# Kernel optimization log

Hardware: AMD Instinct MI355X
Metric: run time of the kernel (lower is better)

The kernel has to match this reference:

```python
import jax, jax.numpy as jnp
import numpy as np

K = 75        # kpoints
L = 8         # number of labels (output_dim)


def _knn_nonconformity(q, t, train_label, k=K, num_labels=L):
    """Brute-force kNN (Euclidean) + distance-weighted nonconformity.
    q: [B, D] queries; t: [N, D] train bank; train_label: [N] int.
    Returns [B, num_labels]: for each class i, sum of 1/dist over the k
    nearest neighbors whose label != i (0 weight for zero distance)."""
    # squared distances [B, N]
    d2 = (jnp.sum(q * q, axis=1, keepdims=True)
          - 2.0 * q @ t.T
          + jnp.sum(t * t, axis=1)[None, :])
    d2 = jnp.maximum(d2, 0.0)
    neg_top, idx = jax.lax.top_k(-d2, k)          # k smallest d2
    dist = jnp.sqrt(jnp.maximum(-neg_top, 0.0))    # [B, k]
    safe = jnp.where(dist > 0, dist, 1.0)
    w = jnp.where(dist > 0, 1.0 / safe, 0.0)       # [B, k]
    mismatch = 1.0 - jax.nn.one_hot(train_label[idx], num_labels, dtype=w.dtype)  # [B,k,L]
    return jnp.einsum('bk,bkl->bl', w, mismatch)


def setup_inputs() -> dict:
    key = jax.random.key(0)
    ks = jax.random.split(key, 12)
    B, N, D, H, C = 1024, 50000, 83, 128, 10000
    s = lambda fan_in: 1.0 / np.sqrt(fan_in)
    return {
        'x': jax.random.normal(ks[0], (B, D), jnp.float32),
        'train_x': jax.random.normal(ks[1], (N, D), jnp.float32),
        'train_label': jax.random.randint(ks[2], (N,), 0, L, jnp.int32),
        'cali': jax.random.uniform(ks[3], (C,), jnp.float32) * 50.0,
        'W1': jax.random.normal(ks[4], (D, H), jnp.float32) * s(D),
        'b1': jnp.zeros((H,), jnp.float32),
        'W2': jax.random.normal(ks[5], (H, H), jnp.float32) * s(H),
        'b2': jnp.zeros((H,), jnp.float32),
        'W3': jax.random.normal(ks[6], (H, H), jnp.float32) * s(H),
        'b3': jnp.zeros((H,), jnp.float32),
        'W4': jax.random.normal(ks[7], (H, L), jnp.float32) * s(H),
        'b4': jnp.zeros((L,), jnp.float32),
    }


def reference(x, train_x, train_label, cali, W1, b1, W2, b2, W3, b3, W4, b4):
    relu = jax.nn.relu
    # query-side MLP (inference: dropout inactive)
    h1 = relu(x @ W1 + b1)
    h2 = relu(h1 @ W2 + b2)
    h3 = relu(h2 @ W3 + b3)
    out = jax.nn.softmax(h3 @ W4 + b4, axis=-1)
    # train-side feature banks (what each kNTree was fit on)
    t1 = relu(train_x @ W1 + b1)
    t2 = relu(t1 @ W2 + b2)
    t3 = relu(t2 @ W3 + b3)
    t4 = jax.nn.softmax(t3 @ W4 + b4, axis=-1)
    # per-layer nonconformity [B, L], summed across the 5 layers
    total = (_knn_nonconformity(x, train_x, train_label)
             + _knn_nonconformity(h1, t1, train_label)
             + _knn_nonconformity(h2, t2, train_label)
             + _knn_nonconformity(h3, t3, train_label)
             + _knn_nonconformity(out, t4, train_label))
    # empirical p-value: fraction of calibration scores >= total nonconformity
    counts = jnp.sum(cali[None, None, :] >= total[:, :, None], axis=-1)  # [B, L]
    return counts.astype(jnp.float32) / cali.shape[0]
```

## Files before the change

### kernel.cpp

```cpp
#include <hip/hip_runtime.h>
#include <math.h>

#define KNN 75
#define NL 8
#define NB 1024
#define NT 50000
#define NT_PAD 50048
#define NCALI 10000
#define KC 32
#define TT 128
#define NTB 391
#define SLOTS 16
#define CAP 6144
#define NSUB 2048
#define NSB 16
#define SSTRIDE 24
#define SOFF 11
#define RSEL 32

#define PB_Q    384
#define PB_BANK 18750
#define PB_W1   48
#define PB_W23  64
#define PREP_BLOCKS (PB_Q+PB_BANK+PB_W1+2*PB_W23)

typedef __attribute__((ext_vector_type(8))) short bf16x8;
typedef __attribute__((ext_vector_type(4))) float f32x4;

__device__ __forceinline__ int swz(int c){ return c + ((c>>5)<<2); }

__device__ __forceinline__ unsigned short f2bf_rn(float x){
  unsigned u = __float_as_uint(x);
  unsigned r = (u + 0x7FFFu + ((u>>16)&1u)) >> 16;
  return (unsigned short)r;
}
__device__ __forceinline__ float bf2f(unsigned short h){
  return __uint_as_float(((unsigned)h)<<16);
}
__device__ __forceinline__ bf16x8 ld8(const unsigned short* p){
  return *(const bf16x8*)p;
}
__device__ __forceinline__ void gl_lds16(const unsigned short* g, unsigned short* l){
  __builtin_amdgcn_global_load_lds(
      (const __attribute__((address_space(1))) void*)g,
      (__attribute__((address_space(3))) void*)l, 16, 0, 0);
}

__device__ __forceinline__ void pad_one(const float* __restrict__ in,
                                        float* __restrict__ out, int M,
                                        int Din, int Dout, int idx){
  if (idx >= M*Dout) return;
  int r = idx / Dout, c = idx - r*Dout;
  out[idx] = (c < Din) ? in[r*Din + c] : 0.f;
}
__device__ __forceinline__ void wsplit_one(const float* __restrict__ W, int kreal,
                                           int dp, unsigned short* __restrict__ WtH,
                                           unsigned short* __restrict__ WtL, int idx){
  int n = idx / dp, k = idx - n*dp;
  float v = (k < kreal) ? W[(size_t)k*128 + n] : 0.f;
  unsigned short h = f2bf_rn(v);
  WtH[idx] = h;
  WtL[idx] = f2bf_rn(v - bf2f(h));
}
__global__ void prep_k(const float* __restrict__ x, float* __restrict__ xq0,
                       const float* __restrict__ txr, float* __restrict__ tbA,
                       const float* __restrict__ W1, unsigned short* wt1H, unsigned short* wt1L,
                       const float* __restrict__ W2, unsigned short* wt2H, unsigned short* wt2L,
                       const float* __restrict__ W3, unsigned short* wt3H, unsigned short* wt3L){
  int b = blockIdx.x, tid = threadIdx.x;
  if (b < PB_Q){
    pad_one(x, xq0, NB, 83, 96, b*256 + tid);
  } else if (b < PB_Q + PB_BANK){
    pad_one(txr, tbA, NT, 83, 96, (b-PB_Q)*256 + tid);
  } else if (b < PB_Q + PB_BANK + PB_W1){
    wsplit_one(W1, 83, 96,  wt1H, wt1L, (b-PB_Q-PB_BANK)*256 + tid);
  } else if (b < PB_Q + PB_BANK + PB_W1 + PB_W23){
    wsplit_one(W2, 128, 128, wt2H, wt2L, (b-PB_Q-PB_BANK-PB_W1)*256 + tid);
  } else {
    wsplit_one(W3, 128, 128, wt3H, wt3L, (b-PB_Q-PB_BANK-PB_W1-PB_W23)*256 + tid);
  }
}

__device__ __forceinline__ void qmlp_layer(
    const float* __restrict__ srcG, int lda,
    float (*H)[132], float (*As)[132], float (*Bs)[148],
    int kchunks, int kreal,
    const float* __restrict__ W, const float* __restrict__ bias,
    float* __restrict__ OutG, int rowBase, int tid)
{
  int r0 = (tid>>4)*8, c0 = (tid&15)*8;
  float acc[8][8];
  #pragma unroll
  for (int i=0;i<8;i++)
    #pragma unroll
    for (int j=0;j<8;j++) acc[i][j]=0.f;

  for (int kc=0;kc<kchunks;kc++){
    { int rr = tid>>3, k4=(tid&7)*4;
      #pragma unroll
      for (int i=0;i<4;i++){
        int row = rr + i*32;
        float4 v;
        if (srcG) v = *(const float4*)&srcG[(size_t)(rowBase+row)*lda + kc*KC + k4];
        else      v = *(const float4*)&H[row][kc*KC + k4];
        As[k4+0][row]=v.x; As[k4+1][row]=v.y; As[k4+2][row]=v.z; As[k4+3][row]=v.w;
      }
    }
    { int kk=tid>>5, c4=(tid&31)*4;
      #pragma unroll
      for (int i=0;i<4;i++){
        int k = kk + i*8, gk = kc*KC + k;
        float4 v = make_float4(0.f,0.f,0.f,0.f);
        if (gk < kreal) v = *(const float4*)&W[(size_t)gk*128 + c4];
        *(float4*)&Bs[k][swz(c4)] = v;
      }
    }
    __syncthreads();
    #pragma unroll 4
    for (int k=0;k<KC;k++){
      float4 a0 = *(const float4*)&As[k][r0];
      float4 a1 = *(const float4*)&As[k][r0+4];
      float4 b0 = *(const float4*)&Bs[k][swz(c0)];
      float4 b1 = *(const float4*)&Bs[k][swz(c0+4)];
      float av[8] = {a0.x,a0.y,a0.z,a0.w,a1.x,a1.y,a1.z,a1.w};
      float bv[8] = {b0.x,b0.y,b0.z,b0.w,b1.x,b1.y,b1.z,b1.w};
      #pragma unroll
      for (int i=0;i<8;i++)
        #pragma unroll
        for (int j=0;j<8;j++) acc[i][j] += av[i]*bv[j];
    }
    __syncthreads();
  }
  float bb[8];
  #pragma unroll
  for (int j=0;j<8;j++) bb[j]=bias[c0+j];
  #pragma unroll
  for (int i=0;i<8;i++){
    int row = r0 + i;
    float o[8];
    #pragma unroll
    for (int j=0;j<8;j++){ float v=acc[i][j]+bb[j]; o[j]=v>0.f?v:0.f; }
    *(float4*)&H[row][c0]   = make_float4(o[0],o[1],o[2],o[3]);
    *(float4*)&H[row][c0+4] = make_float4(o[4],o[5],o[6],o[7]);
    *(float4*)&OutG[(size_t)(rowBase+row)*128 + c0]   = make_float4(o[0],o[1],o[2],o[3]);
    *(float4*)&OutG[(size_t)(rowBase+row)*128 + c0+4] = make_float4(o[4],o[5],o[6],o[7]);
  }
  __syncthreads();
}

__device__ __forceinline__ void qsplit(float (*H)[132],
                                       unsigned short* __restrict__ qh,
                                       unsigned short* __restrict__ ql,
                                       float* __restrict__ qn,
                                       int rowBase, int tid){
  if (tid < 128){
    int gr = rowBase + tid;
    float s = 0.f;
    for (int k=0;k<128;k++){
      float v = H[tid][k];
      s += v*v;
      unsigned short h = f2bf_rn(v);
      qh[(size_t)gr*128 + k] = h;
      ql[(size_t)gr*128 + k] = f2bf_rn(v - bf2f(h));
    }
    qn[gr] = s;
  }
}

__global__ __launch_bounds__(256) void qmlp_k(
    const float* __restrict__ xq0,
    const float* __restrict__ W1, const float* __restrict__ b1,
    const float* __restrict__ W2, const float* __restrict__ b2,
    const float* __restrict__ W3, const float* __restrict__ b3,
    const float* __restrict__ W4, const float* __restrict__ b4,
    float* __restrict__ xq1, float* __restrict__ xq2, float* __restrict__ xq3,
    float* __restrict__ xq4,
    unsigned short* qH1, unsigned short* qL1,
    unsigned short* qH2, unsigned short* qL2,
    unsigned short* qH3, unsigned short* qL3,
    unsigned short* qH4, unsigned short* qL4,
    float* __restrict__ qnb)
{
  __shared__ float As[KC][132];
  __shared__ float Bs[KC][148];
  __shared__ float H[128][132];
  int tid = threadIdx.x;
  int rowBase = blockIdx.x*128;

  qmlp_layer(xq0, 96, H, As, Bs, 3, 83,  W1, b1, xq1, rowBase, tid);
  qsplit(H, qH1, qL1, qnb+1*NB, rowBase, tid);
  qmlp_layer(nullptr, 0, H, As, Bs, 4, 128, W2, b2, xq2, rowBase, tid);
  qsplit(H, qH2, qL2, qnb+2*NB, rowBase, tid);
  qmlp_layer(nullptr, 0, H, As, Bs, 4, 128, W3, b3, xq3, rowBase, tid);
  qsplit(H, qH3, qL3, qnb+3*NB, rowBase, tid);

  float* W4s = (float*)Bs;
  for (int i=tid;i<1024;i+=256) W4s[i]=W4[i];
  __syncthreads();
  if (tid < 128){
    int row = rowBase + tid;
    float v[8];
    #pragma unroll
    for (int c=0;c<8;c++) v[c]=b4[c];
    for (int k=0;k<128;k++){
      float a = H[tid][k];
      #pragma unroll
      for (int c=0;c<8;c++) v[c] += a*W4s[k*8+c];
    }
    float m=-1e30f;
    #pragma unroll
    for (int c=0;c<8;c++) m = v[c]>m ? v[c] : m;
    float s=0.f;
    #pragma unroll
    for (int c=0;c<8;c++){ v[c]=__expf(v[c]-m); s+=v[c]; }
    float inv=1.f/s;
    float* p = &xq4[(size_t)row*32];
    float nn=0.f;
    #pragma unroll
    for (int c=0;c<8;c++){
      float pv = v[c]*inv;
      p[c]=pv;
      nn += pv*pv;
      unsigned short h = f2bf_rn(pv);
      qH4[(size_t)row*32 + c] = h;
      qL4[(size_t)row*32 + c] = f2bf_rn(pv - bf2f(h));
    }
    #pragma unroll
    for (int j=8;j<32;j++){ p[j]=0.f; qH4[(size_t)row*32+j]=0; qL4[(size_t)row*32+j]=0; }
    qnb[4*NB + row] = nn;
  }
}

__global__ void mlp8sm_k(const float* __restrict__ A, const float* __restrict__ W4,
                         const float* __restrict__ b4, float* __restrict__ Out,
                         unsigned short* __restrict__ SH, unsigned short* __restrict__ SL,
                         float* __restrict__ nrm, int M){
  __shared__ float Ws[128*8];
  int tid = threadIdx.x;
  for (int i=tid;i<1024;i+=256) Ws[i]=W4[i];
  __syncthreads();
  int r = blockIdx.x*32 + (tid>>3), c = tid&7;
  if (r >= M) return;
  const float* a = &A[(size_t)r*128];
  float acc = b4[c];
  #pragma unroll 16
  for (int k=0;k<128;k++) acc += a[k]*Ws[k*8+c];
  int lane = tid & 63, base = lane & ~7;
  float v[8];
  #pragma unroll
  for (int j=0;j<8;j++) v[j] = __shfl(acc, base+j, 64);
  float m=-1e30f;
  #pragma unroll
  for (int j=0;j<8;j++) m = v[j]>m ? v[j] : m;
  float s=0.f;
  #pragma unroll
  for (int j=0;j<8;j++){ v[j]=__expf(v[j]-m); s+=v[j]; }
  float inv=1.f/s;
  float nn=0.f;
  #pragma unroll
  for (int j=0;j<8;j++){ float pv=v[j]*inv; v[j]=pv; nn+=pv*pv; }
  float* p = &Out[(size_t)r*32];
  float pv = v[c];
  p[c]    = pv;
  p[8+c]  = 0.f;
  p[16+c] = 0.f;
  p[24+c] = 0.f;
  unsigned short h = f2bf_rn(pv);
  SH[(size_t)r*32 + c]    = h;
  SL[(size_t)r*32 + c]    = f2bf_rn(pv - bf2f(h));
  SH[(size_t)r*32 + 8+c]  = 0; SL[(size_t)r*32 + 8+c]  = 0;
  SH[(size_t)r*32 + 16+c] = 0; SL[(size_t)r*32 + 16+c] = 0;
  SH[(size_t)r*32 + 24+c] = 0; SL[(size_t)r*32 + 24+c] = 0;
  if (c==0) nrm[r] = nn;
}

__global__ void conv_norm_k(
    const float* __restrict__ XA, unsigned short* __restrict__ HA,
    unsigned short* __restrict__ LA, float* __restrict__ nA, int MA,
    const float* __restrict__ XB, unsigned short* __restrict__ HB,
    unsigned short* __restrict__ LB, float* __restrict__ nB, int MB,
    int dp)
{
  int w = threadIdx.x>>6, lane = threadIdx.x&63;
  int row = blockIdx.x*4 + w;
  const float* src; unsigned short* dh; unsigned short* dl; float* nrm;
  if (row < MA){
    src=&XA[(size_t)row*dp]; dh=&HA[(size_t)row*dp]; dl=&LA[(size_t)row*dp]; nrm=&nA[row];
  } else {
    int r2 = row - MA;
    if (r2 >= MB) return;
    src=&XB[(size_t)r2*dp]; dh=&HB[(size_t)r2*dp]; dl=&LB[(size_t)r2*dp]; nrm=&nB[r2];
  }
  float s=0.f;
  for (int c=lane*2; c<dp; c+=128){
    float2 v = *(const float2*)&src[c];
    s += v.x*v.x + v.y*v.y;
    unsigned short h0 = f2bf_rn(v.x), h1 = f2bf_rn(v.y);
    float r0 = v.x - bf2f(h0), r1 = v.y - bf2f(h1);
    ushort2 hh; hh.x=h0; hh.y=h1;
    ushort2 ll; ll.x=f2bf_rn(r0); ll.y=f2bf_rn(r1);
    *(ushort2*)&dh[c]=hh;
    *(ushort2*)&dl[c]=ll;
  }
  #pragma unroll
  for (int off=32;off>0;off>>=1) s += __shfl_down(s, off, 64);
  if (lane==0) *nrm=s;
}

__device__ __forceinline__ void find_bin(int* hist, int* part, int nb, int Krem,
                                         int tid, int* s_B, int* s_lob){
  int ch = nb>>8;
  int base = tid*ch;
  int s=0;
  for (int b=base;b<base+ch;b++) s+=hist[b];
  int lane = tid & 63, wv = tid>>6;
  int v = s;
  #pragma unroll
  for (int off=1; off<64; off<<=1){
    int u = __shfl_up(v, off, 64);
    if (lane >= off) v += u;
  }
  if (lane==63) part[wv] = v;
  __syncthreads();
  int wbase = 0;
  #pragma unroll
  for (int w2=0; w2<4; w2++) wbase += (w2 < wv) ? part[w2] : 0;
  v += wbase;
  int excl = v - s;
  if (v >= Krem && excl < Krem){
    int lob = excl, B = base + ch - 1;
    for (int b=base;b<base+ch;b++){
      if (lob + hist[b] >= Krem){ B=b; break; }
      lob += hist[b];
    }
    *s_B = B; *s_lob = lob;
  }
  if (tid==255 && v < Krem){ *s_B = nb-1; *s_lob = 0; }
  __syncthreads();
}

__global__ __launch_bounds__(256) void sel64_k(const unsigned* __restrict__ skeys,
                                               unsigned* __restrict__ Tthr){
  __shared__ unsigned buf[NSUB];
  __shared__ int hist[2048];
  __shared__ int part[256];
  __shared__ int sB, sLob;
  int tid=threadIdx.x, q=blockIdx.x;
  for (int i=tid;i<NSUB;i+=256) buf[i]=skeys[(size_t)q*NSUB+i];
  int Krem=RSEL;
  for (int i=tid;i<2048;i+=256) hist[i]=0;
  __syncthreads();
  for (int i=tid;i<NSUB;i+=256) atomicAdd(&hist[buf[i]>>21],1);
  __syncthreads();
  find_bin(hist,part,2048,Krem,tid,&sB,&sLob);
  unsigned pre=(unsigned)sB; Krem-=sLob;
  for (int i=tid;i<2048;i+=256) hist[i]=0;
  __syncthreads();
  for (int i=tid;i<NSUB;i+=256){ unsigned k=buf[i]; if ((k>>21)==pre) atomicAdd(&hist[(k>>10)&0x7FFu],1); }
  __syncthreads();
  find_bin(hist,part,2048,Krem,tid,&sB,&sLob);
  pre=(pre<<11)|(unsigned)sB; Krem-=sLob;
  for (int i=tid;i<1024;i+=256) hist[i]=0;
  __syncthreads();
  for (int i=tid;i<NSUB;i+=256){ unsigned k=buf[i]; if ((k>>10)==pre) atomicAdd(&hist[k&0x3FFu],1); }
  __syncthreads();
  find_bin(hist,part,1024,Krem,tid,&sB,&sLob);
  if (tid==0) Tthr[q]=(pre<<10)|(unsigned)sB;
}

#define MFMA_SEC(BHC, BLC, AH, AL)                                               \
  _Pragma("unroll")                                                              \
  for (int tj=0;tj<8;tj++){                                                      \
    int rowB = tj*16 + col;                                                      \
    int sw = (((quad + (rowB>>1)) & 3) << 3);                                    \
    bf16x8 bh = *(const bf16x8*)&(BHC)[rowB*32 + sw];                            \
    bf16x8 bl = *(const bf16x8*)&(BLC)[rowB*32 + sw];                            \
    acc[tj] = __builtin_amdgcn_mfma_f32_16x16x32_bf16(AH, bh, acc[tj], 0,0,0);   \
    acc[tj] = __builtin_amdgcn_mfma_f32_16x16x32_bf16(AH, bl, acc[tj], 0,0,0);   \
    acc[tj] = __builtin_amdgcn_mfma_f32_16x16x32_bf16(AL, bh, acc[tj], 0,0,0);   \
  }

#define MFMA_KLOOP(ROWMAP)                                                       \
  size_t aoff = (size_t)(qbase + w*16 + col)*dp + quad*8;                        \
  const unsigned short* pAH = QH + aoff;                                         \
  const unsigned short* pAL = QL + aoff;                                         \
  int i0 = tid,      row0 = i0>>2, sg0 = ((i0&3) - (row0>>1)) & 3;               \
  int i1 = tid+256,  row1 = i1>>2, sg1 = ((i1&3) - (row1>>1)) & 3;               \
  size_t g0 = (size_t)(ROWMAP(n0+row0))*dp + (size_t)sg0*8;                      \
  size_t g1 = (size_t)(ROWMAP(n0+row1))*dp + (size_t)sg1*8;                      \
  f32x4 acc[8];                                                                  \
  _Pragma("unroll")                                                              \
  for (int tj=0;tj<8;tj++){ f32x4 z={0.f,0.f,0.f,0.f}; acc[tj]=z; }              \
  gl_lds16(TH + g0, BH0 + i0*8);                                                 \
  gl_lds16(TH + g1, BH0 + i1*8);                                                 \
  gl_lds16(TL + g0, BL0 + i0*8);                                                 \
  gl_lds16(TL + g1, BL0 + i1*8);                                                 \
  bf16x8 xh = ld8(pAH), xl = ld8(pAL);                                           \
  bf16x8 yh = xh, yl = xl;                                                       \
  _Pragma("unroll")                                                              \
  for (int kc=0; kc<kchunks; kc+=2){                                             \
    __syncthreads();                                                             \
    if (kc+1 < kchunks){                                                         \
      size_t ko=(size_t)(kc+1)*32;                                               \
      gl_lds16(TH + g0 + ko, BH1 + i0*8);                                        \
      gl_lds16(TH + g1 + ko, BH1 + i1*8);                                        \
      gl_lds16(TL + g0 + ko, BL1 + i0*8);                                        \
      gl_lds16(TL + g1 + ko, BL1 + i1*8);                                        \
      yh = ld8(pAH + ko); yl = ld8(pAL + ko);                                    \
    }                                                                            \
    MFMA_SEC(BH0, BL0, xh, xl);                                                  \
    if (kc+1 < kchunks){                                                         \
      __syncthreads();                                                           \
      if (kc+2 < kchunks){                                                       \
        size_t ko=(size_t)(kc+2)*32;                                             \
        gl_lds16(TH + g0 + ko, BH0 + i0*8);                                      \
        gl_lds16(TH + g1 + ko, BH0 + i1*8);                                      \
        gl_lds16(TL + g0 + ko, BL0 + i0*8);                                      \
        gl_lds16(TL + g1 + ko, BL0 + i1*8);                                      \
        xh = ld8(pAH + ko); xl = ld8(pAL + ko);                                  \
      }                                                                          \
      MFMA_SEC(BH1, BL1, yh, yl);                                                \
    }                                                                            \
  }

#define ROW_ID(r) (r)
#define ROW_SUB(r) ((r)*SSTRIDE + SOFF)

template<int KCH>
__global__ __launch_bounds__(256) void dist_mfma_k(
    const unsigned short* __restrict__ QH, const unsigned short* __restrict__ QL,
    const unsigned short* __restrict__ TH, const unsigned short* __restrict__ TL,
    const float* __restrict__ qn, const float* __restrict__ tn,
    const int* __restrict__ labels, const unsigned* __restrict__ Tthr,
    unsigned* __restrict__ slab)
{
  constexpr int dp = KCH*32;
  __shared__ __align__(16) unsigned short smem[4*4096];
  unsigned short* BH0 = smem;
  unsigned short* BH1 = smem + 4096;
  unsigned short* BL0 = smem + 8192;
  unsigned short* BL1 = smem + 12288;
  unsigned (*hitbuf)[SLOTS] = (unsigned (*)[SLOTS])smem;
  int* hcnt = (int*)(smem + 4096);
  int b = blockIdx.x;
  int xcd = b & 7, s = b >> 3;
  int qb = s & 15, tslot = s >> 4;
  int t_blk = xcd + 8*tslot;
  if (t_blk >= NTB) return;
  int tid = threadIdx.x, w = tid>>6, lane = tid&63;
  int quad = lane>>4, col = lane&15;
  int qbase = qb*64;
  int n0 = t_blk*TT;
  constexpr int kchunks = KCH;

  MFMA_KLOOP(ROW_ID)

  __syncthreads();
  if (tid<64) hcnt[tid]=0;
  __syncthreads();
  float qnr[4]; unsigned Tq[4]; float thrF[4];
  #pragma unroll
  for (int r=0;r<4;r++){
    int q = qbase + w*16 + quad*4 + r;
    qnr[r]  = qn[q];
    Tq[r]   = Tthr[q];
    thrF[r] = __uint_as_float(Tq[r] | 7u);
  }
  #pragma unroll
  for (int tj=0;tj<8;tj++){
    int t = n0 + tj*16 + col;
    if (t < NT){
      float tnv = tn[t];
      unsigned lab = (unsigned)labels[t];
      #pragma unroll
      for (int r=0;r<4;r++){
        float d2 = fmaf(-2.f, acc[tj][r], qnr[r] + tnv);
        if (d2 <= thrF[r]){
          float d2c = fmaxf(d2, 0.f);
          unsigned key = (__float_as_uint(d2c)&0xFFFFFFF8u) | lab;
          if (key < Tq[r]){
            int ql = w*16 + quad*4 + r;
            int idx = atomicAdd(&hcnt[ql], 1);
            if (idx < SLOTS-1) hitbuf[ql][1+idx] = key;
          }
        }
      }
    }
  }
  __syncthreads();
  if (tid<64) hitbuf[tid][0]=(unsigned)hcnt[tid];
  __syncthreads();
  {
    int q = tid>>2, sub = (tid&3)*4;
    uint4 v = *(uint4*)&hitbuf[q][sub];
    *(uint4*)&slab[((size_t)(qbase+q)*NTB + t_blk)*SLOTS + sub] = v;
  }
}

template<int KCH>
__global__ __launch_bounds__(256) void dist_sub_k(
    const unsigned short* __restrict__ QH, const unsigned short* __restrict__ QL,
    const unsigned short* __restrict__ TH, const unsigned short* __restrict__ TL,
    const float* __restrict__ qn, const float* __restrict__ tn,
    const int* __restrict__ labels, unsigned* __restrict__ keys)
{
  constexpr int dp = KCH*32;
  __shared__ __align__(16) unsigned short smem[4*4096];
  unsigned short* BH0 = smem;
  unsigned short* BH1 = smem + 4096;
  unsigned short* BL0 = smem + 8192;
  unsigned short* BL1 = smem + 12288;
  int b = blockIdx.x;
  int qb = b & 15, t_blk = b >> 4;
  int tid = threadIdx.x, w = tid>>6, lane = tid&63;
  int quad = lane>>4, col = lane&15;
  int qbase = qb*64;
  int n0 = t_blk*TT;
  constexpr int kchunks = KCH;

  MFMA_KLOOP(ROW_SUB)

  float qnr[4];
  #pragma unroll
  for (int r=0;r<4;r++)
    qnr[r] = qn[qbase + w*16 + quad*4 + r];
  #pragma unroll
  for (int tj=0;tj<8;tj++){
    int sI = n0 + tj*16 + col;
    int g  = sI*SSTRIDE + SOFF;
    float tnv = tn[g];
    unsigned lab = (unsigned)labels[g];
    #pragma unroll
    for (int r=0;r<4;r++){
      float d2 = fmaxf(fmaf(-2.f, acc[tj][r], qnr[r] + tnv), 0.f);
      unsigned key = (__float_as_uint(d2)&0xFFFFFFF8u) | lab;
      int q = qbase + w*16 + quad*4 + r;
      keys[(size_t)q*NSUB + sI] = key;
    }
  }
}

template<int KCH>
__global__ __launch_bounds__(256) void mlp_mfma_k(
    const unsigned short* __restrict__ QH, const unsigned short* __restrict__ QL,
    const unsigned short* __restrict__ TH, const unsigned short* __restrict__ TL,
    const float* __restrict__ bias, float* __restrict__ Out,
    unsigned short* __restrict__ SH, unsigned short* __restrict__ SL,
    float* __restrict__ nrm, int M)
{
  constexpr int dp = KCH*32;
  __shared__ __align__(16) unsigned short smem[4*4096];
  unsigned short* BH0 = smem;
  unsigned short* BH1 = smem + 4096;
  unsigned short* BL0 = smem + 8192;
  unsigned short* BL1 = smem + 12288;
  int tid = threadIdx.x, w = tid>>6, lane = tid&63;
  int quad = lane>>4, col = lane&15;
  int qbase = blockIdx.x*64;
  int n0 = 0;
  constexpr int kchunks = KCH;

  MFMA_KLOOP(ROW_ID)

  float bb[8];
  #pragma unroll
  for (int tj=0;tj<8;tj++) bb[tj] = bias[tj*16 + col];
  #pragma unroll
  for (int r=0;r<4;r++){
    int row = qbase + w*16 + quad*4 + r;
    if (row < M){
      float vv[8]; float s=0.f;
      #pragma unroll
      for (int tj=0;tj<8;tj++){
        float v = acc[tj][r] + bb[tj];
        v = v > 0.f ? v : 0.f;
        vv[tj] = v;
        s += v*v;
        Out[(size_t)row*128 + tj*16 + col] = v;
      }
      #pragma unroll
      for (int off=1; off<16; off<<=1) s += __shfl_xor(s, off, 16);
      if (col==0) nrm[row] = s;
      #pragma unroll
      for (int tj=0;tj<8;tj++){
        unsigned short h = f2bf_rn(vv[tj]);
        SH[(size_t)row*128 + tj*16 + col] = h;
        SL[(size_t)row*128 + tj*16 + col] = f2bf_rn(vv[tj] - bf2f(h));
      }
    }
  }
}

__global__ __launch_bounds__(256) void final_k(
    const unsigned* __restrict__ slab,
    const float* __restrict__ Qm, const float* __restrict__ Tm,
    const float* __restrict__ qn, const float* __restrict__ tn,
    const int* __restrict__ labels,
    float* __restrict__ tot, int first, int dp)
{
  __shared__ int hist[2048];
  __shared__ int part[256];
  __shared__ unsigned buf[CAP];
  __shared__ unsigned lowbuf[96];
  __shared__ float qrow[128];
  __shared__ int sB,sLob,s_cnt,s_low,s_bad;
  __shared__ float s_w[9];
  int tid=threadIdx.x, q=blockIdx.x;
  if (tid==0){ for (int j=0;j<9;j++) s_w[j]=0.f; s_cnt=0; s_low=0; s_bad=0; }
  __syncthreads();

  const unsigned* sq = slab + (size_t)q*NTB*SLOTS;
  for (int sidx=tid; sidx<NTB; sidx+=256){
    const unsigned* s = sq + (size_t)sidx*SLOTS;
    uint4 a = *(const uint4*)s;
    unsigned cnt = a.x;
    if (cnt > SLOTS-1){ s_bad=1; continue; }
    if (!cnt) continue;
    int base = atomicAdd(&s_cnt, (int)cnt);
    if (base + (int)cnt <= CAP){
      buf[base] = a.y;
      if (cnt>=2) buf[base+1] = a.z;
      if (cnt>=3) buf[base+2] = a.w;
      for (unsigned w=4; w<=cnt; w++) buf[base+w-1] = s[w];
    }
  }
  __syncthreads();
  int total = s_cnt;
  int bad = s_bad;

#define CONTRIB(kk) do{ float d2_=__uint_as_float((kk)&0xFFFFFFF8u); \
    if (d2_>0.f){ float w_=1.0f/sqrtf(d2_); \
      atomicAdd(&s_w[8],w_); atomicAdd(&s_w[(kk)&7u],w_); } }while(0)

  unsigned T; int Krem=KNN;
  if (!bad && total>=KNN && total<=CAP){
    for (int i=tid;i<2048;i+=256) hist[i]=0;
    __syncthreads();
    for (int i=tid;i<total;i+=256) atomicAdd(&hist[buf[i]>>21],1);
    __syncthreads();
    find_bin(hist,part,2048,Krem,tid,&sB,&sLob);
    unsigned pre=(unsigned)sB; Krem-=sLob;
    for (int i=tid;i<2048;i+=256) hist[i]=0;
    __syncthreads();
    for (int i=tid;i<total;i+=256){ unsigned k=buf[i]; if ((k>>21)==pre) atomicAdd(&hist[(k>>10)&0x7FFu],1); }
    __syncthreads();
    find_bin(hist,part,2048,Krem,tid,&sB,&sLob);
    pre=(pre<<11)|(unsigned)sB; Krem-=sLob;
    for (int i=tid;i<1024;i+=256) hist[i]=0;
    __syncthreads();
    for (int i=tid;i<total;i+=256){ unsigned k=buf[i]; if ((k>>10)==pre) atomicAdd(&hist[k&0x3FFu],1); }
    __syncthreads();
    find_bin(hist,part,1024,Krem,tid,&sB,&sLob);
    T=(pre<<10)|(unsigned)sB; Krem-=sLob;
    __syncthreads();
    for (int i=tid;i<total;i+=256){ unsigned k=buf[i]; if (k<T) CONTRIB(k); }
  } else {
    if (tid==0) s_cnt=0;
    for (int i=tid;i<dp;i+=256) qrow[i]=Qm[(size_t)q*dp+i];
    __syncthreads();
    float qq=qn[q];
    auto KEY=[&](int t)->unsigned{
      const float* br=&Tm[(size_t)t*dp];
      float dot=0.f;
      for (int k2=0;k2<dp;k2++) dot+=qrow[k2]*br[k2];
      float d2=fmaxf(qq-2.f*dot+tn[t],0.f);
      return (__float_as_uint(d2)&0xFFFFFFF8u)|(unsigned)labels[t];
    };
    for (int i=tid;i<2048;i+=256) hist[i]=0;
    __syncthreads();
    for (int t=tid;t<NT;t+=256) atomicAdd(&hist[KEY(t)>>21],1);
    __syncthreads();
    find_bin(hist,part,2048,Krem,tid,&sB,&sLob);
    int c=hist[sB]; Krem-=sLob;
    unsigned prefix=(unsigned)sB; int shift=21;
    if (c > CAP){
      __syncthreads();
      for (int i=tid;i<2048;i+=256) hist[i]=0;
      __syncthreads();
      for (int t=tid;t<NT;t+=256){ unsigned k=KEY(t); if ((k>>21)==prefix) atomicAdd(&hist[(k>>10)&0x7FFu],1); }
      __syncthreads();
      find_bin(hist,part,2048,Krem,tid,&sB,&sLob);
      c=hist[sB]; Krem-=sLob; prefix=(prefix<<11)|(unsigned)sB; shift=10;
    }
    if (c > CAP){
      __syncthreads();
      for (int i=tid;i<1024;i+=256) hist[i]=0;
      __syncthreads();
      for (int t=tid;t<NT;t+=256){ unsigned k=KEY(t); if ((k>>10)==prefix) atomicAdd(&hist[k&0x3FFu],1); }
      __syncthreads();
      find_bin(hist,part,1024,Krem,tid,&sB,&sLob);
      c=hist[sB]; Krem-=sLob; prefix=(prefix<<10)|(unsigned)sB; shift=0;
    }
    if (c <= CAP){
      for (int t=tid;t<NT;t+=256){
        unsigned k=KEY(t); unsigned pp=k>>shift;
        if (pp==prefix){ int j=atomicAdd(&s_cnt,1); if (j<CAP) buf[j]=k; }
        else if (pp<prefix){ int j=atomicAdd(&s_low,1); if (j<96) lowbuf[j]=k; }
      }
      __syncthreads();
      int sh=shift;
      while (sh>0){
        int nsh=(sh==21)?10:0;
        int nb=1<<(sh-nsh);
        __syncthreads();
        for (int i=tid;i<nb;i+=256) hist[i]=0;
        __syncthreads();
        int cc=s_cnt;
        for (int i=tid;i<cc;i+=256) atomicAdd(&hist[(buf[i]>>nsh)&(unsigned)(nb-1)],1);
        __syncthreads();
        find_bin(hist,part,nb,Krem,tid,&sB,&sLob);
        Krem-=sLob; prefix=(prefix<<(sh-nsh))|(unsigned)sB; sh=nsh;
      }
      T=prefix;
      __syncthreads();
      int lowc=s_low, cc=s_cnt;
      for (int i=tid;i<lowc;i+=256){ unsigned k=lowbuf[i]; CONTRIB(k); }
      for (int i=tid;i<cc;i+=256){ unsigned k=buf[i]; if (k<T) CONTRIB(k); }
    } else {
      T=prefix;
      for (int t=tid;t<NT;t+=256){ unsigned k=KEY(t); if (k<T) CONTRIB(k); }
    }
  }
  __syncthreads();
  if (tid==0){
    float d2=__uint_as_float(T&0xFFFFFFF8u);
    float w=(d2>0.f)?(1.0f/sqrtf(d2)):0.f;
    s_w[8] += (float)Krem*w;
    s_w[T&7u] += (float)Krem*w;
  }
  __syncthreads();
  if (tid<8){
    float contrib = s_w[8]-s_w[tid];
    size_t o=(size_t)q*NL+tid;
    tot[o] = first ? contrib : tot[o]+contrib;
  }
#undef CONTRIB
}

__global__ void pvalue_k(const float* __restrict__ tot, const float* __restrict__ cali,
                         float* __restrict__ out){
  __shared__ float t8[NL];
  __shared__ int part[4][NL];
  int tid=threadIdx.x, q=blockIdx.x;
  if (tid<NL) t8[tid]=tot[(size_t)q*NL+tid];
  __syncthreads();
  float th[NL];
  #pragma unroll
  for (int c=0;c<NL;c++) th[c]=t8[c];
  int cnt[NL];
  #pragma unroll
  for (int c=0;c<NL;c++) cnt[c]=0;
  for (int i=tid;i<NCALI;i+=256){
    float v=cali[i];
    #pragma unroll
    for (int c=0;c<NL;c++) cnt[c] += (v>=th[c]) ? 1 : 0;
  }
  #pragma unroll
  for (int c=0;c<NL;c++){
    #pragma unroll
    for (int off=32;off>0;off>>=1) cnt[c]+=__shfl_down(cnt[c],off,64);
  }
  if ((tid&63)==0){
    #pragma unroll
    for (int c=0;c<NL;c++) part[tid>>6][c]=cnt[c];
  }
  __syncthreads();
  if (tid<NL){
    int s=part[0][tid]+part[1][tid]+part[2][tid]+part[3][tid];
    out[(size_t)q*NL+tid] = (float)s / 10000.f;
  }
}

template<int KCH>
static void knn_layer(const float* Qm, const float* Bank,
                      const unsigned short* qh, const unsigned short* ql, float* qnl,
                      const unsigned short* bkH, const unsigned short* bkL,
                      int first, const int* lbl, float* tnb,
                      unsigned* skeys, unsigned* sT, unsigned* slab,
                      float* tot, hipStream_t stream){
  constexpr int dp = KCH*32;
  dist_sub_k<KCH><<<16*NSB,256,0,stream>>>(qh,ql,bkH,bkL,qnl,tnb,lbl,skeys);
  sel64_k<<<NB,256,0,stream>>>(skeys,sT);
  dist_mfma_k<KCH><<<8*16*49,256,0,stream>>>(qh,ql,bkH,bkL,qnl,tnb,lbl,sT,slab);
  final_k<<<NB,256,0,stream>>>(slab,Qm,Bank,qnl,tnb,lbl,tot,first,dp);
}

extern "C" void kernel_launch(void* const* d_in, const int* in_sizes, int n_in,
                              void* d_out, int out_size, void* d_ws, size_t ws_size,
                              hipStream_t stream) {
  const float* x   = (const float*)d_in[0];
  const float* txr = (const float*)d_in[1];
  const int*   lbl = (const int*)  d_in[2];
  const float* cal = (const float*)d_in[3];
  const float* W1  = (const float*)d_in[4];
  const float* b1  = (const float*)d_in[5];
  const float* W2  = (const float*)d_in[6];
  const float* b2  = (const float*)d_in[7];
  const float* W3  = (const float*)d_in[8];
  const float* b3  = (const float*)d_in[9];
  const float* W4  = (const float*)d_in[10];
  const float* b4  = (const float*)d_in[11];
  float* out = (float*)d_out;
  float* ws  = (float*)d_ws;

  size_t off=0;
  float* xq0=ws+off; off+=(size_t)NB*96;
  float* xq1=ws+off; off+=(size_t)NB*128;
  float* xq2=ws+off; off+=(size_t)NB*128;
  float* xq3=ws+off; off+=(size_t)NB*128;
  float* xq4=ws+off; off+=(size_t)NB*32;
  float* tbA=ws+off; off+=(size_t)NT*128;
  float* tbB=ws+off; off+=(size_t)NT*128;
  float* tb4=ws+off; off+=(size_t)NT*32;
  float* qnb=ws+off; off+=(size_t)5*NB;
  float* tnb=ws+off; off+=(size_t)NT;
  float* tot=ws+off; off+=(size_t)NB*NL;
  unsigned* sT=(unsigned*)(ws+off); off+=NB;
  unsigned short* qH0=(unsigned short*)(ws+off); off+=(size_t)NB*48;
  unsigned short* qL0=(unsigned short*)(ws+off); off+=(size_t)NB*48;
  unsigned short* qH1=(unsigned short*)(ws+off); off+=(size_t)NB*64;
  unsigned short* qL1=(unsigned short*)(ws+off); off+=(size_t)NB*64;
  unsigned short* qH2=(unsigned short*)(ws+off); off+=(size_t)NB*64;
  unsigned short* qL2=(unsigned short*)(ws+off); off+=(size_t)NB*64;
  unsigned short* qH3=(unsigned short*)(ws+off); off+=(size_t)NB*64;
  unsigned short* qL3=(unsigned short*)(ws+off); off+=(size_t)NB*64;
  unsigned short* qH4=(unsigned short*)(ws+off); off+=(size_t)NB*16;
  unsigned short* qL4=(unsigned short*)(ws+off); off+=(size_t)NB*16;
  unsigned short* bkAH=(unsigned short*)(ws+off); off+=(size_t)NT_PAD*64;
  unsigned short* bkAL=(unsigned short*)(ws+off); off+=(size_t)NT_PAD*64;
  unsigned short* bkBH=(unsigned short*)(ws+off); off+=(size_t)NT_PAD*64;
  unsigned short* bkBL=(unsigned short*)(ws+off); off+=(size_t)NT_PAD*64;
  unsigned short* wt1H=(unsigned short*)(ws+off); off+=(size_t)128*48;
  unsigned short* wt1L=(unsigned short*)(ws+off); off+=(size_t)128*48;
  unsigned short* wt2H=(unsigned short*)(ws+off); off+=(size_t)128*64;
  unsigned short* wt2L=(unsigned short*)(ws+off); off+=(size_t)128*64;
  unsigned short* wt3H=(unsigned short*)(ws+off); off+=(size_t)128*64;
  unsigned short* wt3L=(unsigned short*)(ws+off); off+=(size_t)128*64;
  off=(off+3)&~(size_t)3;
  unsigned* slab=(unsigned*)(ws+off);
  unsigned* skeys=(unsigned*)(ws+off);
  { size_t slab_sz=(size_t)NB*NTB*SLOTS, skey_sz=(size_t)NB*NSUB;
    off += (slab_sz > skey_sz ? slab_sz : skey_sz); }

  prep_k<<<PREP_BLOCKS,256,0,stream>>>(x,xq0,txr,tbA,
                                       W1,wt1H,wt1L,W2,wt2H,wt2L,W3,wt3H,wt3L);
  qmlp_k<<<8,256,0,stream>>>(xq0,W1,b1,W2,b2,W3,b3,W4,b4,xq1,xq2,xq3,xq4,
                             qH1,qL1,qH2,qL2,qH3,qL3,qH4,qL4,qnb);
  conv_norm_k<<<(NT+NB)/4,256,0,stream>>>(tbA, bkAH, bkAL, tnb, NT,
                                          xq0, qH0, qL0, qnb+0*NB, NB, 96);

  knn_layer<3>(xq0, tbA, qH0,qL0, qnb+0*NB, bkAH,bkAL, 1, lbl, tnb, skeys,sT,slab, tot, stream);
  mlp_mfma_k<3><<<2*NTB,256,0,stream>>>(bkAH,bkAL,wt1H,wt1L,b1,tbB,bkBH,bkBL,tnb,NT);
  knn_layer<4>(xq1, tbB, qH1,qL1, qnb+1*NB, bkBH,bkBL, 0, lbl, tnb, skeys,sT,slab, tot, stream);
  mlp_mfma_k<4><<<2*NTB,256,0,stream>>>(bkBH,bkBL,wt2H,wt2L,b2,tbA,bkAH,bkAL,tnb,NT);
  knn_layer<4>(xq2, tbA, qH2,qL2, qnb+2*NB, bkAH,bkAL, 0, lbl, tnb, skeys,sT,slab, tot, stream);
  mlp_mfma_k<4><<<2*NTB,256,0,stream>>>(bkAH,bkAL,wt3H,wt3L,b3,tbB,bkBH,bkBL,tnb,NT);
  knn_layer<4>(xq3, tbB, qH3,qL3, qnb+3*NB, bkBH,bkBL, 0, lbl, tnb, skeys,sT,slab, tot, stream);
  mlp8sm_k<<<(NT+31)/32,256,0,stream>>>(tbB,W4,b4,tb4,bkAH,bkAL,tnb,NT);
  knn_layer<1>(xq4, tb4, qH4,qL4, qnb+4*NB, bkAH,bkAL, 0, lbl, tnb, skeys,sT,slab, tot, stream);

  pvalue_k<<<NB,256,0,stream>>>(tot,cal,out);
}
```

Baseline: 725.8 us.

## Fold query-side MLP into bank MLP kernels, drop serial qmlp kernel

Removes the standalone 8-block qmlp_k kernel that computed the query MLP layers in fp32 with little parallelism. Extra blocks are appended to each bank-side mlp_mfma_k launch and to mlp8sm_k, so the query rows go through the same split-bf16 MFMA path. This takes a low-occupancy serial kernel off the critical path. The query MLP now depends on the bf16 hi/lo split of the previous layer's outputs, and the final layer's query handling and output layout may not match what qmlp_k used to write.

```diff
diff --git a/kernel.cpp b/kernel.cpp
--- a/kernel.cpp
+++ b/kernel.cpp
@@ -17,6 +17,7 @@
 #define SSTRIDE 24
 #define SOFF 11
 #define RSEL 32
+#define MLP8_BQ 1563
 
 #define PB_Q    384
 #define PB_BANK 18750
@@ -81,166 +82,28 @@
   }
 }
 
-__device__ __forceinline__ void qmlp_layer(
-    const float* __restrict__ srcG, int lda,
-    float (*H)[132], float (*As)[132], float (*Bs)[148],
-    int kchunks, int kreal,
-    const float* __restrict__ W, const float* __restrict__ bias,
-    float* __restrict__ OutG, int rowBase, int tid)
-{
-  int r0 = (tid>>4)*8, c0 = (tid&15)*8;
-  float acc[8][8];
-  #pragma unroll
-  for (int i=0;i<8;i++)
-    #pragma unroll
-    for (int j=0;j<8;j++) acc[i][j]=0.f;
-
-  for (int kc=0;kc<kchunks;kc++){
-    { int rr = tid>>3, k4=(tid&7)*4;
-      #pragma unroll
-      for (int i=0;i<4;i++){
-        int row = rr + i*32;
-        float4 v;
-        if (srcG) v = *(const float4*)&srcG[(size_t)(rowBase+row)*lda + kc*KC + k4];
-        else      v = *(const float4*)&H[row][kc*KC + k4];
-        As[k4+0][row]=v.x; As[k4+1][row]=v.y; As[k4+2][row]=v.z; As[k4+3][row]=v.w;
-      }
-    }
-    { int kk=tid>>5, c4=(tid&31)*4;
-      #pragma unroll
-      for (int i=0;i<4;i++){
-        int k = kk + i*8, gk = kc*KC + k;
-        float4 v = make_float4(0.f,0.f,0.f,0.f);
-        if (gk < kreal) v = *(const float4*)&W[(size_t)gk*128 + c4];
-        *(float4*)&Bs[k][swz(c4)] = v;
-      }
-    }
-    __syncthreads();
-    #pragma unroll 4
-    for (int k=0;k<KC;k++){
-      float4 a0 = *(const float4*)&As[k][r0];
-      float4 a1 = *(const float4*)&As[k][r0+4];
-      float4 b0 = *(const float4*)&Bs[k][swz(c0)];
-      float4 b1 = *(const float4*)&Bs[k][swz(c0+4)];
-      float av[8] = {a0.x,a0.y,a0.z,a0.w,a1.x,a1.y,a1.z,a1.w};
-      float bv[8] = {b0.x,b0.y,b0.z,b0.w,b1.x,b1.y,b1.z,b1.w};
-      #pragma unroll
-      for (int i=0;i<8;i++)
-        #pragma unroll
-        for (int j=0;j<8;j++) acc[i][j] += av[i]*bv[j];
-    }
-    __syncthreads();
-  }
-  float bb[8];
-  #pragma unroll
-  for (int j=0;j<8;j++) bb[j]=bias[c0+j];
-  #pragma unroll
-  for (int i=0;i<8;i++){
-    int row = r0 + i;
-    float o[8];
-    #pragma unroll
-    for (int j=0;j<8;j++){ float v=acc[i][j]+bb[j]; o[j]=v>0.f?v:0.f; }
-    *(float4*)&H[row][c0]   = make_float4(o[0],o[1],o[2],o[3]);
-    *(float4*)&H[row][c0+4] = make_float4(o[4],o[5],o[6],o[7]);
-    *(float4*)&OutG[(size_t)(rowBase+row)*128 + c0]   = make_float4(o[0],o[1],o[2],o[3]);
-    *(float4*)&OutG[(size_t)(rowBase+row)*128 + c0+4] = make_float4(o[4],o[5],o[6],o[7]);
-  }
-  __syncthreads();
-}
-
-__device__ __forceinline__ void qsplit(float (*H)[132],
-                                       unsigned short* __restrict__ qh,
-                                       unsigned short* __restrict__ ql,
-                                       float* __restrict__ qn,
-                                       int rowBase, int tid){
-  if (tid < 128){
-    int gr = rowBase + tid;
-    float s = 0.f;
-    for (int k=0;k<128;k++){
-      float v = H[tid][k];
-      s += v*v;
-      unsigned short h = f2bf_rn(v);
-      qh[(size_t)gr*128 + k] = h;
-      ql[(size_t)gr*128 + k] = f2bf_rn(v - bf2f(h));
-    }
-    qn[gr] = s;
-  }
-}
-
-__global__ __launch_bounds__(256) void qmlp_k(
-    const float* __restrict__ xq0,
-    const float* __restrict__ W1, const float* __restrict__ b1,
-    const float* __restrict__ W2, const float* __restrict__ b2,
-    const float* __restrict__ W3, const float* __restrict__ b3,
-    const float* __restrict__ W4, const float* __restrict__ b4,
-    float* __restrict__ xq1, float* __restrict__ xq2, float* __restrict__ xq3,
-    float* __restrict__ xq4,
-    unsigned short* qH1, unsigned short* qL1,
-    unsigned short* qH2, unsigned short* qL2,
-    unsigned short* qH3, unsigned short* qL3,
-    unsigned short* qH4, unsigned short* qL4,
-    float* __restrict__ qnb)
-{
-  __shared__ float As[KC][132];
-  __shared__ float Bs[KC][148];
-  __shared__ float H[128][132];
-  int tid = threadIdx.x;
-  int rowBase = blockIdx.x*128;
-
-  qmlp_layer(xq0, 96, H, As, Bs, 3, 83,  W1, b1, xq1, rowBase, tid);
-  qsplit(H, qH1, qL1, qnb+1*NB, rowBase, tid);
-  qmlp_layer(nullptr, 0, H, As, Bs, 4, 128, W2, b2, xq2, rowBase, tid);
-  qsplit(H, qH2, qL2, qnb+2*NB, rowBase, tid);
-  qmlp_layer(nullptr, 0, H, As, Bs, 4, 128, W3, b3, xq3, rowBase, tid);
-  qsplit(H, qH3, qL3, qnb+3*NB, rowBase, tid);
-
-  float* W4s = (float*)Bs;
-  for (int i=tid;i<1024;i+=256) W4s[i]=W4[i];
-  __syncthreads();
-  if (tid < 128){
-    int row = rowBase + tid;
-    float v[8];
-    #pragma unroll
-    for (int c=0;c<8;c++) v[c]=b4[c];
-    for (int k=0;k<128;k++){
-      float a = H[tid][k];
-      #pragma unroll
-      for (int c=0;c<8;c++) v[c] += a*W4s[k*8+c];
-    }
-    float m=-1e30f;
-    #pragma unroll
-    for (int c=0;c<8;c++) m = v[c]>m ? v[c] : m;
-    float s=0.f;
-    #pragma unroll
-    for (int c=0;c<8;c++){ v[c]=__expf(v[c]-m); s+=v[c]; }
-    float inv=1.f/s;
-    float* p = &xq4[(size_t)row*32];
-    float nn=0.f;
-    #pragma unroll
-    for (int c=0;c<8;c++){
-      float pv = v[c]*inv;
-      p[c]=pv;
-      nn += pv*pv;
-      unsigned short h = f2bf_rn(pv);
-      qH4[(size_t)row*32 + c] = h;
-      qL4[(size_t)row*32 + c] = f2bf_rn(pv - bf2f(h));
-    }
-    #pragma unroll
-    for (int j=8;j<32;j++){ p[j]=0.f; qH4[(size_t)row*32+j]=0; qL4[(size_t)row*32+j]=0; }
-    qnb[4*NB + row] = nn;
-  }
-}
-
-__global__ void mlp8sm_k(const float* __restrict__ A, const float* __restrict__ W4,
-                         const float* __restrict__ b4, float* __restrict__ Out,
-                         unsigned short* __restrict__ SH, unsigned short* __restrict__ SL,
-                         float* __restrict__ nrm, int M){
+__global__ void mlp8sm_k(const float* __restrict__ AB, const float* __restrict__ AQ,
+                         const float* __restrict__ W4, const float* __restrict__ b4,
+                         float* __restrict__ OutB,
+                         unsigned short* __restrict__ SBH, unsigned short* __restrict__ SBL,
+                         float* __restrict__ nrmB,
+                         float* __restrict__ OutQ,
+                         unsigned short* __restrict__ SQH, unsigned short* __restrict__ SQL,
+                         float* __restrict__ nrmQ){
   __shared__ float Ws[128*8];
   int tid = threadIdx.x;
   for (int i=tid;i<1024;i+=256) Ws[i]=W4[i];
   __syncthreads();
-  int r = blockIdx.x*32 + (tid>>3), c = tid&7;
+  int b = blockIdx.x;
+  bool isq = (b >= MLP8_BQ);
+  int r = (isq ? (b-MLP8_BQ) : b)*32 + (tid>>3), c = tid&7;
+  int M = isq ? NB : NT;
   if (r >= M) return;
+  const float* A = isq ? AQ : AB;
+  float* Out = isq ? OutQ : OutB;
+  unsigned short* SH = isq ? SQH : SBH;
+  unsigned short* SL = isq ? SQL : SBL;
+  float* nrm = isq ? nrmQ : nrmB;
   const float* a = &A[(size_t)r*128];
   float acc = b4[c];
   #pragma unroll 16
@@ -542,11 +405,14 @@
 
 template<int KCH>
 __global__ __launch_bounds__(256) void mlp_mfma_k(
-    const unsigned short* __restrict__ QH, const unsigned short* __restrict__ QL,
+    const unsigned short* __restrict__ bkH, const unsigned short* __restrict__ bkL,
+    const unsigned short* __restrict__ qh,  const unsigned short* __restrict__ ql,
     const unsigned short* __restrict__ TH, const unsigned short* __restrict__ TL,
-    const float* __restrict__ bias, float* __restrict__ Out,
-    unsigned short* __restrict__ SH, unsigned short* __restrict__ SL,
-    float* __restrict__ nrm, int M)
+    const float* __restrict__ bias,
+    float* __restrict__ OutB, unsigned short* __restrict__ SBH,
+    unsigned short* __restrict__ SBL, float* __restrict__ nrmB,
+    float* __restrict__ OutQ, unsigned short* __restrict__ SQH,
+    unsigned short* __restrict__ SQL, float* __restrict__ nrmQ)
 {
   constexpr int dp = KCH*32;
   __shared__ __align__(16) unsigned short smem[4*4096];
@@ -554,9 +420,18 @@
   unsigned short* BH1 = smem + 4096;
   unsigned short* BL0 = smem + 8192;
   unsigned short* BL1 = smem + 12288;
+  int b = blockIdx.x;
+  bool isq = (b >= 2*NTB);
+  const unsigned short* QH = isq ? qh : bkH;
+  const unsigned short* QL = isq ? ql : bkL;
+  float* Out = isq ? OutQ : OutB;
+  unsigned short* SH = isq ? SQH : SBH;
+  unsigned short* SL = isq ? SQL : SBL;
+  float* nrm = isq ? nrmQ : nrmB;
+  int M = isq ? NB : NT;
   int tid = threadIdx.x, w = tid>>6, lane = tid&63;
   int quad = lane>>4, col = lane&15;
-  int qbase = blockIdx.x*64;
+  int qbase = (isq ? (b - 2*NTB) : b) * 64;
   int n0 = 0;
   constexpr int kchunks = KCH;
 
@@ -844,19 +719,21 @@
 
   prep_k<<<PREP_BLOCKS,256,0,stream>>>(x,xq0,txr,tbA,
                                        W1,wt1H,wt1L,W2,wt2H,wt2L,W3,wt3H,wt3L);
-  qmlp_k<<<8,256,0,stream>>>(xq0,W1,b1,W2,b2,W3,b3,W4,b4,xq1,xq2,xq3,xq4,
-                             qH1,qL1,qH2,qL2,qH3,qL3,qH4,qL4,qnb);
   conv_norm_k<<<(NT+NB)/4,256,0,stream>>>(tbA, bkAH, bkAL, tnb, NT,
                                           xq0, qH0, qL0, qnb+0*NB, NB, 96);
 
   knn_layer<3>(xq0, tbA, qH0,qL0, qnb+0*NB, bkAH,bkAL, 1, lbl, tnb, skeys,sT,slab, tot, stream);
-  mlp_mfma_k<3><<<2*NTB,256,0,stream>>>(bkAH,bkAL,wt1H,wt1L,b1,tbB,bkBH,bkBL,tnb,NT);
+  mlp_mfma_k<3><<<2*NTB+16,256,0,stream>>>(bkAH,bkAL, qH0,qL0, wt1H,wt1L, b1,
+                                           tbB,bkBH,bkBL,tnb, xq1,qH1,qL1,qnb+1*NB);
   knn_layer<4>(xq1, tbB, qH1,qL1, qnb+1*NB, bkBH,bkBL, 0, lbl, tnb, skeys,sT,slab, tot, stream);
-  mlp_mfma_k<4><<<2*NTB,256,0,stream>>>(bkBH,bkBL,wt2H,wt2L,b2,tbA,bkAH,bkAL,tnb,NT);
+  mlp_mfma_k<4><<<2*NTB+16,256,0,stream>>>(bkBH,bkBL, qH1,qL1, wt2H,wt2L, b2,
+                                           tbA,bkAH,bkAL,tnb, xq2,qH2,qL2,qnb+2*NB);
   knn_layer<4>(xq2, tbA, qH2,qL2, qnb+2*NB, bkAH,bkAL, 0, lbl, tnb, skeys,sT,slab, tot, stream);
-  mlp_mfma_k<4><<<2*NTB,256,0,stream>>>(bkAH,bkAL,wt3H,wt3L,b3,tbB,bkBH,bkBL,tnb,NT);
+  mlp_mfma_k<4><<<2*NTB+16,256,0,stream>>>(bkAH,bkAL, qH2,qL2, wt3H,wt3L, b3,
+                                           tbB,bkBH,bkBL,tnb, xq3,qH3,qL3,qnb+3*NB);
   knn_layer<4>(xq3, tbB, qH3,qL3, qnb+3*NB, bkBH,bkBL, 0, lbl, tnb, skeys,sT,slab, tot, stream);
-  mlp8sm_k<<<(NT+31)/32,256,0,stream>>>(tbB,W4,b4,tb4,bkAH,bkAL,tnb,NT);
+  mlp8sm_k<<<MLP8_BQ+32,256,0,stream>>>(tbB, xq3, W4, b4,
+                                        tb4,bkAH,bkAL,tnb, xq4,qH4,qL4,qnb+4*NB);
   knn_layer<1>(xq4, tb4, qH4,qL4, qnb+4*NB, bkAH,bkAL, 0, lbl, tnb, skeys,sT,slab, tot, stream);
 
   pvalue_k<<<NB,256,0,stream>>>(tot,cal,out);
```

Result: faster. 647.6 us (-10.8%).
